# Kernel tuning notes

Hardware: AMD Instinct MI355X
Metric: run time of the kernel (lower is better)

Reference implementation:

```python
import jax, jax.numpy as jnp
import numpy as np

H = 16      # query heads
KV = 4      # kv heads
HD = 128    # head dim
THETA = 10000.0
NEG = -1e9


def _rope_tables(S, dtype):
    inv_freq = 1.0 / (THETA ** (jnp.arange(0, HD, 2, dtype=jnp.float32) / HD))
    ang = jnp.arange(S, dtype=jnp.float32)[:, None] * inv_freq[None, :]  # [S, HD/2]
    emb = jnp.concatenate([ang, ang], axis=-1)  # [S, HD]
    return jnp.cos(emb).astype(dtype), jnp.sin(emb).astype(dtype)


def _rotate_half(x):
    x1, x2 = jnp.split(x, 2, axis=-1)
    return jnp.concatenate([-x2, x1], axis=-1)


def _apply_rope(t, cos, sin):
    # t: [B, h, S, HD]; cos/sin: [S, HD]
    return t * cos[None, None] + _rotate_half(t) * sin[None, None]


def setup_inputs() -> dict:
    key = jax.random.key(0)
    ks = jax.random.split(key, 5)
    B, S, D = 2, 2048, 2048
    sc = 0.02
    return {
        "x": jax.random.normal(ks[0], (B, S, D), jnp.float32),
        "wq": jax.random.normal(ks[1], (D, D), jnp.float32) * sc,
        "wk": jax.random.normal(ks[2], (KV * HD, D), jnp.float32) * sc,
        "wv": jax.random.normal(ks[3], (KV * HD, D), jnp.float32) * sc,
        "wo": jax.random.normal(ks[4], (D, D), jnp.float32) * sc,
    }


def reference(x, wq, wk, wv, wo):
    B, S, D = x.shape
    q = (x @ wq.T).reshape(B, S, H, HD).transpose(0, 2, 1, 3)   # [B,H,S,HD]
    k = (x @ wk.T).reshape(B, S, KV, HD).transpose(0, 2, 1, 3)  # [B,KV,S,HD]
    v = (x @ wv.T).reshape(B, S, KV, HD).transpose(0, 2, 1, 3)

    cos, sin = _rope_tables(S, x.dtype)
    q = _apply_rope(q, cos, sin)
    k = _apply_rope(k, cos, sin)

    # GQA: repeat kv heads to match query heads (q_group_num = H // KV)
    k = jnp.repeat(k, H // KV, axis=1)  # [B,H,S,HD]
    v = jnp.repeat(v, H // KV, axis=1)

    scores = jnp.einsum("bhqd,bhkd->bhqk", q, k) / jnp.sqrt(jnp.float32(HD)).astype(x.dtype)
    causal = jnp.where(jnp.tril(jnp.ones((S, S), bool)), 0.0, NEG).astype(jnp.float32)
    attn = jax.nn.softmax(scores.astype(jnp.float32) + causal, axis=-1).astype(x.dtype)

    out = jnp.einsum("bhqk,bhkd->bhqd", attn, v)  # [B,H,S,HD]
    out = out.transpose(0, 2, 1, 3).reshape(B, S, D)
    return out @ wo.T
```

## Files before the change

kernel.cpp:

```cpp
#include <hip/hip_runtime.h>
#include <math.h>

typedef unsigned short u16;
typedef __attribute__((ext_vector_type(8))) short short8;
typedef __attribute__((ext_vector_type(8))) __bf16 bf16x8;
typedef __attribute__((ext_vector_type(4))) float floatx4;
typedef __attribute__((ext_vector_type(16))) float floatx16;
typedef __attribute__((ext_vector_type(4))) unsigned short u16x4;
typedef __attribute__((ext_vector_type(4))) float float4v;
typedef __attribute__((ext_vector_type(4))) unsigned int uint4v;

static __device__ __forceinline__ float b2f(u16 u) {
  unsigned int x = ((unsigned int)u) << 16;
  return __builtin_bit_cast(float, x);
}
static __device__ __forceinline__ u16 f2b(float f) {
  unsigned int x = __builtin_bit_cast(unsigned int, f);
  x += 0x7fffu + ((x >> 16) & 1u);
  return (u16)(x >> 16);
}
static __device__ __forceinline__ unsigned int pk2(float lo, float hi) {
  unsigned int r;
  asm("v_cvt_pk_bf16_f32 %0, %1, %2" : "=v"(r) : "v"(lo), "v"(hi));
  return r;
}
static __device__ __forceinline__ float max3f(float a, float b, float c) {
  return fmaxf(fmaxf(a, b), c);
}
static __device__ __forceinline__ void gload_lds16(const void* g, void* l) {
  __builtin_amdgcn_global_load_lds(
      (const __attribute__((address_space(1))) unsigned int*)g,
      (__attribute__((address_space(3))) unsigned int*)l, 16, 0, 0);
}

__global__ __launch_bounds__(256) void cvt5_kernel(
    const float* __restrict__ x, const float* __restrict__ wq,
    const float* __restrict__ wk, const float* __restrict__ wv,
    const float* __restrict__ wo, u16* __restrict__ xb, u16* __restrict__ wqb,
    u16* __restrict__ wkb, u16* __restrict__ wvb, u16* __restrict__ wob) {
  int bid = blockIdx.x;
  const float* in;
  u16* out;
  int i0;
  if (bid < 8192) { in = x; out = xb; i0 = bid; }
  else if (bid < 12288) { in = wq; out = wqb; i0 = bid - 8192; }
  else if (bid < 13312) { in = wk; out = wkb; i0 = bid - 12288; }
  else if (bid < 14336) { in = wv; out = wvb; i0 = bid - 13312; }
  else { in = wo; out = wob; i0 = bid - 14336; }
  int i = i0 * 256 + threadIdx.x;
  float4v v = reinterpret_cast<const float4v*>(in)[i];
  u16x4 o;
  o[0] = f2b(v[0]); o[1] = f2b(v[1]); o[2] = f2b(v[2]); o[3] = f2b(v[3]);
  reinterpret_cast<u16x4*>(out)[i] = o;
}

__global__ __launch_bounds__(256) void rope_table_kernel(float* __restrict__ ct,
                                                         float* __restrict__ st) {
  int idx = blockIdx.x * 256 + threadIdx.x;
  int s = idx >> 6, j = idx & 63;
  float inv = powf(10000.0f, -(float)j * (1.0f / 64.0f));
  float ang = (float)s * inv;
  ct[idx] = cosf(ang);
  st[idx] = sinf(ang);
}

__global__ __launch_bounds__(256) void kvprep_kernel(const u16* __restrict__ in,
                                                     u16* __restrict__ kr,
                                                     u16* __restrict__ vtb,
                                                     const float* __restrict__ ct,
                                                     const float* __restrict__ st) {
  __shared__ u16 t[128][66];
  if (blockIdx.x < 512) {
    int idx = blockIdx.x * 256 + threadIdx.x;
    int jc = idx & 7;
    int rest = idx >> 3;
    int h = rest & 3;
    int bs = rest >> 2;
    int s = bs & 2047;
    int b = bs >> 11;
    int j0 = jc * 8;
    size_t inoff = (size_t)bs * 3072 + 2048 + h * 128 + j0;
    short8 lo = *reinterpret_cast<const short8*>(&in[inoff]);
    short8 hi = *reinterpret_cast<const short8*>(&in[inoff + 64]);
    short8 o0, o1;
#pragma unroll
    for (int e = 0; e < 8; ++e) {
      float c = ct[s * 64 + j0 + e], sn = st[s * 64 + j0 + e];
      float t1 = b2f((u16)lo[e]);
      float t2 = b2f((u16)hi[e]);
      o0[e] = (short)f2b(t1 * c - t2 * sn);
      o1[e] = (short)f2b(t2 * c + t1 * sn);
    }
    size_t ooff = ((size_t)(b * 4 + h) * 2048 + s) * 128 + j0;
    *reinterpret_cast<short8*>(&kr[ooff]) = o0;
    *reinterpret_cast<short8*>(&kr[ooff + 64]) = o1;
  } else {
    int vb = blockIdx.x - 512;
    int s0 = (vb & 31) * 64;
    int by = vb >> 5;
    int b = by >> 2, kv = by & 3;
    int tid = threadIdx.x;
#pragma unroll
    for (int it = 0; it < 32; ++it) {
      int idx = it * 256 + tid;
      int sl = idx >> 7, d = idx & 127;
      t[d][sl] = in[(size_t)(b * 2048 + s0 + sl) * 3072 + 2560 + kv * 128 + d];
    }
    __syncthreads();
#pragma unroll
    for (int it = 0; it < 32; ++it) {
      int idx = it * 256 + tid;
      int d = idx >> 6, sl = idx & 63;
      vtb[(size_t)((b * 4 + kv) * 128 + d) * 2048 + s0 + sl] = t[d][sl];
    }
  }
}

static __device__ __forceinline__ void store_out(u16* p, float v) { *p = f2b(v); }
static __device__ __forceinline__ void store_out(float* p, float v) { *p = v; }

template <typename OutT>
__global__ __launch_bounds__(256) void gemm_bt(const u16* __restrict__ A,
                                               const u16* __restrict__ B,
                                               OutT* __restrict__ C, int M, int N, int K) {
  __shared__ __align__(16) u16 Al[3][128 * 32];
  __shared__ __align__(16) u16 Bl[3][128 * 32];
  const int tid = threadIdx.x;
  const int lane = tid & 63;
  const int w = tid >> 6;
  const int wr = w >> 1, wc = w & 1;
  const int lr = lane & 15, lg = lane >> 4;
  const int brow = blockIdx.y, bcol = blockIdx.x;
  const int r0 = lane >> 2, kp = lane & 3;
  const u16* Ag = A + (size_t)(brow * 128) * K;
  const u16* Bg = B + (size_t)(bcol * 128) * K;
  floatx4 acc[4][4] = {};
  const int NT = K >> 5;

  auto stage = [&](int buf, int t) {
#pragma unroll
    for (int j = 0; j < 2; ++j) {
      int c = w * 2 + j;
      int row = c * 16 + r0;
      gload_lds16(Ag + (size_t)row * K + t * 32 + kp * 8, &Al[buf][c * 512]);
      gload_lds16(Bg + (size_t)row * K + t * 32 + kp * 8, &Bl[buf][c * 512]);
    }
  };

  stage(0, 0);
  stage(1, 1);
  asm volatile("s_waitcnt vmcnt(4)\n\ts_barrier" ::: "memory");

  int cur = 0, nxt = 2;
  for (int t = 0; t < NT; ++t) {
    if (t + 2 < NT) stage(nxt, t + 2);
    bf16x8 af[4], bfr[4];
#pragma unroll
    for (int m = 0; m < 4; ++m)
      af[m] = *reinterpret_cast<const bf16x8*>(&Al[cur][(wr * 64 + m * 16 + lr) * 32 + lg * 8]);
#pragma unroll
    for (int n = 0; n < 4; ++n)
      bfr[n] = *reinterpret_cast<const bf16x8*>(&Bl[cur][(wc * 64 + n * 16 + lr) * 32 + lg * 8]);
    __builtin_amdgcn_s_setprio(1);
#pragma unroll
    for (int m = 0; m < 4; ++m)
#pragma unroll
      for (int n = 0; n < 4; ++n)
        acc[m][n] = __builtin_amdgcn_mfma_f32_16x16x32_bf16(af[m], bfr[n], acc[m][n], 0, 0, 0);
    __builtin_amdgcn_s_setprio(0);
    if (t + 2 < NT) {
      asm volatile("s_waitcnt vmcnt(4)\n\ts_barrier" ::: "memory");
    } else if (t + 1 < NT) {
      asm volatile("s_waitcnt vmcnt(0)\n\ts_barrier" ::: "memory");
    }
    cur = (cur == 2) ? 0 : cur + 1;
    nxt = (nxt == 2) ? 0 : nxt + 1;
  }
#pragma unroll
  for (int m = 0; m < 4; ++m) {
    int row = brow * 128 + wr * 64 + m * 16 + lg * 4;
#pragma unroll
    for (int n = 0; n < 4; ++n) {
      int col = bcol * 128 + wc * 64 + n * 16 + lr;
#pragma unroll
      for (int i = 0; i < 4; ++i) store_out(&C[(size_t)(row + i) * N + col], acc[m][n][i]);
    }
  }
}

__global__ __launch_bounds__(256, 2) void attn_kernel(
    const u16* __restrict__ QKV, const u16* __restrict__ K,
    const u16* __restrict__ V, const float* __restrict__ ct,
    const float* __restrict__ st, u16* __restrict__ O, u16* __restrict__ Opart,
    float* __restrict__ Mpart, float* __restrict__ Lpart) {
  __shared__ __align__(16) u16 Kl[2][64 * 128];
  __shared__ __align__(16) u16 Vl[2][128 * 64];
  const int tid = threadIdx.x, lane = tid & 63, w = tid >> 6;
  const int ql = lane & 31, h2 = lane >> 5;
  const int idx = blockIdx.x;
  const int bh = idx & 31, pp = (idx >> 5) & 7, half = idx >> 8;
  const int b = bh >> 4, hh = bh & 15, kv = hh >> 2;
  const int t_l = 15 - pp, t_s = pp;
  const int pidx = bh * 8 + pp;
  const u16* Kp = K + (size_t)(b * 4 + kv) * 2048 * 128;
  const u16* Vp = V + (size_t)(b * 4 + kv) * 128 * 2048;
  const float cl = 0.08838834764831845f * 1.44269504088896f;
  const uint4v ones_u = {0x3F803F80u, 0x3F803F80u, 0x3F803F80u, 0x3F803F80u};
  const bf16x8 ones = __builtin_bit_cast(bf16x8, ones_u);

  auto stage = [&](int buf, int kb) {
#pragma unroll
    for (int j = 0; j < 4; ++j) {
      int slot = j * 256 + tid;
      int row = slot >> 4, d16 = slot & 15;
      gload_lds16(Kp + (size_t)(kb * 64 + row) * 128 + (d16 ^ (row & 15)) * 8,
                  &Kl[buf][(j * 256 + w * 64) * 8]);
      int d = slot >> 3, k8 = slot & 7;
      gload_lds16(Vp + (size_t)d * 2048 + kb * 64 + (k8 ^ (d & 7)) * 8,
                  &Vl[buf][(j * 256 + w * 64) * 8]);
    }
  };

  auto run_segment = [&](int t, int kvs, int kve, int part) {
    const int q0w = t * 128 + w * 32;
    const int qg = q0w + ql;
    bf16x8 qa[8];
    {
      const u16* qp = QKV + ((size_t)(b * 2048 + qg)) * 3072 + hh * 128;
      short8 rr[8];
#pragma unroll
      for (int dk = 0; dk < 8; ++dk)
        rr[dk] = *reinterpret_cast<const short8*>(qp + dk * 16 + h2 * 8);
      const float* cb = ct + (size_t)qg * 64;
      const float* sb = st + (size_t)qg * 64;
#pragma unroll
      for (int dk = 0; dk < 4; ++dk) {
        short8 olo, ohi;
#pragma unroll
        for (int e = 0; e < 8; ++e) {
          int j = dk * 16 + h2 * 8 + e;
          float c = cb[j] * cl, sn = sb[j] * cl;
          float t1 = b2f((u16)rr[dk][e]);
          float t2 = b2f((u16)rr[dk + 4][e]);
          olo[e] = (short)f2b(t1 * c - t2 * sn);
          ohi[e] = (short)f2b(t2 * c + t1 * sn);
        }
        qa[dk] = __builtin_bit_cast(bf16x8, olo);
        qa[dk + 4] = __builtin_bit_cast(bf16x8, ohi);
      }
    }
    float m_r = -1e30f;
    floatx16 oacc[4] = {};
    floatx16 lsum = {};
    stage(0, kvs);
    __syncthreads();
    int cur = 0;
    for (int kb = kvs; kb < kve; ++kb) {
      if (kb + 1 < kve) stage(cur ^ 1, kb + 1);
      if (kb * 64 <= q0w + 31) {
        const u16* Klc = Kl[cur];
        const u16* Vlc = Vl[cur];
        floatx16 sT0 = {}, sT1 = {};
        __builtin_amdgcn_s_setprio(1);
#pragma unroll
        for (int dk = 0; dk < 8; ++dk) {
          int row0 = ql, row1 = 32 + ql;
          bf16x8 ak0 = *reinterpret_cast<const bf16x8*>(
              &Klc[row0 * 128 + (((dk * 2 + h2) ^ (row0 & 15))) * 8]);
          bf16x8 ak1 = *reinterpret_cast<const bf16x8*>(
              &Klc[row1 * 128 + (((dk * 2 + h2) ^ (row1 & 15))) * 8]);
          sT0 = __builtin_amdgcn_mfma_f32_32x32x16_bf16(ak0, qa[dk], sT0, 0, 0, 0);
          sT1 = __builtin_amdgcn_mfma_f32_32x32x16_bf16(ak1, qa[dk], sT1, 0, 0, 0);
        }
        __builtin_amdgcn_s_setprio(0);
        float x[32];
        const bool domask = (kb * 64 + 63 > q0w);
#pragma unroll
        for (int rg = 0; rg < 16; ++rg) {
          int kloc0 = (rg & 3) + 8 * (rg >> 2) + 4 * h2;
          float v0 = sT0[rg];
          float v1 = sT1[rg];
          if (domask) {
            if (kb * 64 + kloc0 > qg) v0 = -1e30f;
            if (kb * 64 + 32 + kloc0 > qg) v1 = -1e30f;
          }
          x[rg] = v0;
          x[16 + rg] = v1;
        }
        float mx[16];
#pragma unroll
        for (int i = 0; i < 16; ++i) mx[i] = fmaxf(x[i], x[i + 16]);
        float y0 = max3f(mx[0], mx[1], mx[2]);
        float y1 = max3f(mx[3], mx[4], mx[5]);
        float y2 = max3f(mx[6], mx[7], mx[8]);
        float y3 = max3f(mx[9], mx[10], mx[11]);
        float y4 = max3f(mx[12], mx[13], mx[14]);
        float tmax = fmaxf(max3f(y0, y1, y2), max3f(y3, y4, mx[15]));
        tmax = fmaxf(tmax, __shfl_xor(tmax, 32));
        if (!__all(tmax - m_r <= 11.0f)) {
          float mn = fmaxf(m_r, tmax);
          float al = exp2f(m_r - mn);
          m_r = mn;
#pragma unroll
          for (int rg = 0; rg < 16; ++rg) {
            int rowq = (rg & 3) + 8 * (rg >> 2) + 4 * h2;
            float arow = __shfl(al, rowq);
            oacc[0][rg] *= arow; oacc[1][rg] *= arow;
            oacc[2][rg] *= arow; oacc[3][rg] *= arow;
            lsum[rg] *= arow;
          }
        }
        float p[32];
#pragma unroll
        for (int i = 0; i < 32; ++i) p[i] = exp2f(x[i] - m_r);
        bf16x8 pa[4];
#pragma unroll
        for (int ka = 0; ka < 2; ++ka) {
          const int o = ka * 16;
          unsigned int x0 = pk2(p[o + 0], p[o + 1]);
          unsigned int x1 = pk2(p[o + 2], p[o + 3]);
          unsigned int y0u = pk2(p[o + 4], p[o + 5]);
          unsigned int y1u = pk2(p[o + 6], p[o + 7]);
          asm volatile("v_permlane32_swap_b32 %0, %1" : "+v"(x0), "+v"(y0u));
          asm volatile("v_permlane32_swap_b32 %0, %1" : "+v"(x1), "+v"(y1u));
          uint4v f0 = {x0, x1, y0u, y1u};
          pa[ka * 2] = __builtin_bit_cast(bf16x8, f0);
          unsigned int z0 = pk2(p[o + 8], p[o + 9]);
          unsigned int z1 = pk2(p[o + 10], p[o + 11]);
          unsigned int u0 = pk2(p[o + 12], p[o + 13]);
          unsigned int u1 = pk2(p[o + 14], p[o + 15]);
          asm volatile("v_permlane32_swap_b32 %0, %1" : "+v"(z0), "+v"(u0));
          asm volatile("v_permlane32_swap_b32 %0, %1" : "+v"(z1), "+v"(u1));
          uint4v f1 = {z0, z1, u0, u1};
          pa[ka * 2 + 1] = __builtin_bit_cast(bf16x8, f1);
        }
        __builtin_amdgcn_s_setprio(1);
#pragma unroll
        for (int tb = 0; tb < 4; ++tb) {
          int d = tb * 32 + ql;
#pragma unroll
          for (int ks = 0; ks < 4; ++ks) {
            bf16x8 bv = *reinterpret_cast<const bf16x8*>(
                &Vlc[d * 64 + (((ks * 2 + h2) ^ (d & 7))) * 8]);
            oacc[tb] = __builtin_amdgcn_mfma_f32_32x32x16_bf16(pa[ks], bv, oacc[tb], 0, 0, 0);
          }
        }
#pragma unroll
        for (int ks = 0; ks < 4; ++ks)
          lsum = __builtin_amdgcn_mfma_f32_32x32x16_bf16(pa[ks], ones, lsum, 0, 0, 0);
        __builtin_amdgcn_s_setprio(0);
      }
      __syncthreads();
      cur ^= 1;
    }
    if (part < 0) {
#pragma unroll
      for (int rg = 0; rg < 16; ++rg) {
        int rowq = (rg & 3) + 8 * (rg >> 2) + 4 * h2;
        float inv = 1.0f / lsum[rg];
        int qrow = t * 128 + w * 32 + rowq;
        size_t base = ((size_t)(b * 2048 + qrow)) * 2048 + hh * 128 + ql;
#pragma unroll
        for (int tb = 0; tb < 4; ++tb)
          O[base + tb * 32] = f2b(oacc[tb][rg] * inv);
      }
    } else {
      size_t pb = ((size_t)(part * 256 + pidx)) * 128;
#pragma unroll
      for (int rg = 0; rg < 16; ++rg) {
        int rowq = (rg & 3) + 8 * (rg >> 2) + 4 * h2;
        size_t base = (pb + w * 32 + rowq) * 128 + ql;
#pragma unroll
        for (int tb = 0; tb < 4; ++tb)
          Opart[base + tb * 32] = f2b(oacc[tb][rg]);
      }
      if (h2 == 0) {
        Mpart[pb + w * 32 + ql] = m_r;
      }
      if (ql == 0) {
#pragma unroll
        for (int rg = 0; rg < 16; ++rg) {
          int rowq = (rg & 3) + 8 * (rg >> 2) + 4 * h2;
          Lpart[pb + w * 32 + rowq] = lsum[rg];
        }
      }
    }
  };

  if (half == 0) {
    run_segment(t_l, 0, 17, 0);
  } else {
    run_segment(t_l, 17, 2 * t_l + 2, 1);
    run_segment(t_s, 0, 2 * t_s + 2, -1);
  }
}

__global__ __launch_bounds__(256) void combine_kernel(
    const u16* __restrict__ Opart, const float* __restrict__ Mpart,
    const float* __restrict__ Lpart, u16* __restrict__ O) {
  int pidx = blockIdx.x;
  int bh = pidx >> 3, pp = pidx & 7;
  int b = bh >> 4, hh = bh & 15;
  int t_l = 15 - pp;
  int tid = threadIdx.x;
  int row = tid >> 1, colbase = (tid & 1) * 64;
  size_t pb0 = (size_t)pidx * 128 + row;
  size_t pb1 = (size_t)(256 + pidx) * 128 + row;
  float m0 = Mpart[pb0], m1 = Mpart[pb1];
  float l0 = Lpart[pb0], l1 = Lpart[pb1];
  float M = fmaxf(m0, m1);
  float w0 = exp2f(m0 - M), w1 = exp2f(m1 - M);
  float inv = 1.0f / (w0 * l0 + w1 * l1);
  size_t ob = ((size_t)(b * 2048 + t_l * 128 + row)) * 2048 + hh * 128 + colbase;
#pragma unroll
  for (int k = 0; k < 8; ++k) {
    short8 o0 = *reinterpret_cast<const short8*>(&Opart[pb0 * 128 + colbase + k * 8]);
    short8 o1 = *reinterpret_cast<const short8*>(&Opart[pb1 * 128 + colbase + k * 8]);
    short8 r;
#pragma unroll
    for (int e = 0; e < 8; ++e)
      r[e] = (short)f2b((w0 * b2f((u16)o0[e]) + w1 * b2f((u16)o1[e])) * inv);
    *reinterpret_cast<short8*>(&O[ob + k * 8]) = r;
  }
}

extern "C" void kernel_launch(void* const* d_in, const int* in_sizes, int n_in,
                              void* d_out, int out_size, void* d_ws, size_t ws_size,
                              hipStream_t stream) {
  const float* x  = (const float*)d_in[0];
  const float* wq = (const float*)d_in[1];
  const float* wk = (const float*)d_in[2];
  const float* wv = (const float*)d_in[3];
  const float* wo = (const float*)d_in[4];
  float* out = (float*)d_out;
  char* ws = (char*)d_ws;
  size_t off = 0;
  auto alloc = [&](size_t bytes) -> void* {
    void* p = ws + off;
    off = (off + bytes + 255) & ~(size_t)255;
    return p;
  };
  u16* xb   = (u16*)alloc(4096ull * 2048 * 2);
  u16* wqb  = (u16*)alloc(2048ull * 2048 * 2);
  u16* wkb  = (u16*)alloc(512ull * 2048 * 2);
  u16* wvb  = (u16*)alloc(512ull * 2048 * 2);
  u16* wob  = (u16*)alloc(2048ull * 2048 * 2);
  u16* qkv  = (u16*)alloc(4096ull * 3072 * 2);
  u16* kr   = (u16*)alloc(4096ull * 512 * 2);
  u16* vtb  = (u16*)alloc(4096ull * 512 * 2);
  float* ctab = (float*)alloc(2048ull * 64 * 4);
  float* stab = (float*)alloc(2048ull * 64 * 4);
  u16* opart  = (u16*)alloc(2ull * 256 * 128 * 128 * 2);
  float* mpart = (float*)alloc(2ull * 256 * 128 * 4);
  float* lpart = (float*)alloc(2ull * 256 * 128 * 4);
  u16* attnb = xb;
  (void)in_sizes; (void)n_in; (void)out_size; (void)ws_size;

  cvt5_kernel<<<18432, 256, 0, stream>>>(x, wq, wk, wv, wo, xb, wqb, wkb, wvb, wob);
  rope_table_kernel<<<512, 256, 0, stream>>>(ctab, stab);

  gemm_bt<u16><<<dim3(24, 32), 256, 0, stream>>>(xb, wqb, qkv, 4096, 3072, 2048);

  kvprep_kernel<<<768, 256, 0, stream>>>(qkv, kr, vtb, ctab, stab);

  attn_kernel<<<dim3(512), 256, 0, stream>>>(qkv, kr, vtb, ctab, stab, attnb,
                                             opart, mpart, lpart);
  combine_kernel<<<dim3(256), 256, 0, stream>>>(opart, mpart, lpart, attnb);

  gemm_bt<float><<<dim3(16, 32), 256, 0, stream>>>(attnb, wob, out, 4096, 2048, 2048);
}
```

Measured before the change: 216.9 us.

## Software-pipeline PV MFMA behind next QK and fold rope table into convert kernel

The attention loop now defers the P·V MFMAs of each KV block to the next iteration, so they are issued after the next block's QK^T MFMAs and can overlap the softmax VALU work. V gets a third LDS buffer so the deferred block's V tile stays valid while the next tile is staged. Separately, the rope table computation is merged into the conversion kernel as extra blocks, removing one launch. The cost is more LDS per block (which may reduce occupancy from the requested 2 blocks/CU) and extra registers held for the pending P fragments.

```diff
diff --git a/kernel.cpp b/kernel.cpp
--- a/kernel.cpp
+++ b/kernel.cpp
@@ -37,8 +37,18 @@
     const float* __restrict__ x, const float* __restrict__ wq,
     const float* __restrict__ wk, const float* __restrict__ wv,
     const float* __restrict__ wo, u16* __restrict__ xb, u16* __restrict__ wqb,
-    u16* __restrict__ wkb, u16* __restrict__ wvb, u16* __restrict__ wob) {
+    u16* __restrict__ wkb, u16* __restrict__ wvb, u16* __restrict__ wob,
+    float* __restrict__ ct, float* __restrict__ st) {
   int bid = blockIdx.x;
+  if (bid >= 18432) {
+    int idx = (bid - 18432) * 256 + threadIdx.x;
+    int s = idx >> 6, j = idx & 63;
+    float inv = powf(10000.0f, -(float)j * (1.0f / 64.0f));
+    float ang = (float)s * inv;
+    ct[idx] = cosf(ang);
+    st[idx] = sinf(ang);
+    return;
+  }
   const float* in;
   u16* out;
   int i0;
@@ -52,16 +62,6 @@
   u16x4 o;
   o[0] = f2b(v[0]); o[1] = f2b(v[1]); o[2] = f2b(v[2]); o[3] = f2b(v[3]);
   reinterpret_cast<u16x4*>(out)[i] = o;
-}
-
-__global__ __launch_bounds__(256) void rope_table_kernel(float* __restrict__ ct,
-                                                         float* __restrict__ st) {
-  int idx = blockIdx.x * 256 + threadIdx.x;
-  int s = idx >> 6, j = idx & 63;
-  float inv = powf(10000.0f, -(float)j * (1.0f / 64.0f));
-  float ang = (float)s * inv;
-  ct[idx] = cosf(ang);
-  st[idx] = sinf(ang);
 }
 
 __global__ __launch_bounds__(256) void kvprep_kernel(const u16* __restrict__ in,
@@ -194,7 +194,7 @@
     const float* __restrict__ st, u16* __restrict__ O, u16* __restrict__ Opart,
     float* __restrict__ Mpart, float* __restrict__ Lpart) {
   __shared__ __align__(16) u16 Kl[2][64 * 128];
-  __shared__ __align__(16) u16 Vl[2][128 * 64];
+  __shared__ __align__(16) u16 Vl[3][128 * 64];
   const int tid = threadIdx.x, lane = tid & 63, w = tid >> 6;
   const int ql = lane & 31, h2 = lane >> 5;
   const int idx = blockIdx.x;
@@ -208,16 +208,18 @@
   const uint4v ones_u = {0x3F803F80u, 0x3F803F80u, 0x3F803F80u, 0x3F803F80u};
   const bf16x8 ones = __builtin_bit_cast(bf16x8, ones_u);
 
-  auto stage = [&](int buf, int kb) {
+  auto stage = [&](int kb) {
+    u16* KlB = Kl[kb & 1];
+    u16* VlB = Vl[kb % 3];
 #pragma unroll
     for (int j = 0; j < 4; ++j) {
       int slot = j * 256 + tid;
       int row = slot >> 4, d16 = slot & 15;
       gload_lds16(Kp + (size_t)(kb * 64 + row) * 128 + (d16 ^ (row & 15)) * 8,
-                  &Kl[buf][(j * 256 + w * 64) * 8]);
+                  &KlB[(j * 256 + w * 64) * 8]);
       int d = slot >> 3, k8 = slot & 7;
       gload_lds16(Vp + (size_t)d * 2048 + kb * 64 + (k8 ^ (d & 7)) * 8,
-                  &Vl[buf][(j * 256 + w * 64) * 8]);
+                  &VlB[(j * 256 + w * 64) * 8]);
     }
   };
 
@@ -252,15 +254,36 @@
     float m_r = -1e30f;
     floatx16 oacc[4] = {};
     floatx16 lsum = {};
-    stage(0, kvs);
+    bf16x8 paP[4];
+    bool have_prev = false;
+    int vprev = 0;
+
+    auto pv_apply = [&](const u16* Vlc) {
+      __builtin_amdgcn_s_setprio(1);
+#pragma unroll
+      for (int tb = 0; tb < 4; ++tb) {
+        int d = tb * 32 + ql;
+#pragma unroll
+        for (int ks = 0; ks < 4; ++ks) {
+          bf16x8 bv = *reinterpret_cast<const bf16x8*>(
+              &Vlc[d * 64 + (((ks * 2 + h2) ^ (d & 7))) * 8]);
+          oacc[tb] = __builtin_amdgcn_mfma_f32_32x32x16_bf16(paP[ks], bv, oacc[tb], 0, 0, 0);
+        }
+      }
+#pragma unroll
+      for (int ks = 0; ks < 4; ++ks)
+        lsum = __builtin_amdgcn_mfma_f32_32x32x16_bf16(paP[ks], ones, lsum, 0, 0, 0);
+      __builtin_amdgcn_s_setprio(0);
+    };
+
+    stage(kvs);
     __syncthreads();
-    int cur = 0;
     for (int kb = kvs; kb < kve; ++kb) {
-      if (kb + 1 < kve) stage(cur ^ 1, kb + 1);
-      if (kb * 64 <= q0w + 31) {
-        const u16* Klc = Kl[cur];
-        const u16* Vlc = Vl[cur];
-        floatx16 sT0 = {}, sT1 = {};
+      if (kb + 1 < kve) stage(kb + 1);
+      const bool doCur = (kb * 64 <= q0w + 31);
+      floatx16 sT0 = {}, sT1 = {};
+      if (doCur) {
+        const u16* Klc = Kl[kb & 1];
         __builtin_amdgcn_s_setprio(1);
 #pragma unroll
         for (int dk = 0; dk < 8; ++dk) {
@@ -273,6 +296,9 @@
           sT1 = __builtin_amdgcn_mfma_f32_32x32x16_bf16(ak1, qa[dk], sT1, 0, 0, 0);
         }
         __builtin_amdgcn_s_setprio(0);
+      }
+      if (have_prev) pv_apply(Vl[vprev]);
+      if (doCur) {
         float x[32];
         const bool domask = (kb * 64 + 63 > q0w);
 #pragma unroll
@@ -313,7 +339,6 @@
         float p[32];
 #pragma unroll
         for (int i = 0; i < 32; ++i) p[i] = exp2f(x[i] - m_r);
-        bf16x8 pa[4];
 #pragma unroll
         for (int ka = 0; ka < 2; ++ka) {
           const int o = ka * 16;
@@ -324,7 +349,7 @@
           asm volatile("v_permlane32_swap_b32 %0, %1" : "+v"(x0), "+v"(y0u));
           asm volatile("v_permlane32_swap_b32 %0, %1" : "+v"(x1), "+v"(y1u));
           uint4v f0 = {x0, x1, y0u, y1u};
-          pa[ka * 2] = __builtin_bit_cast(bf16x8, f0);
+          paP[ka * 2] = __builtin_bit_cast(bf16x8, f0);
           unsigned int z0 = pk2(p[o + 8], p[o + 9]);
           unsigned int z1 = pk2(p[o + 10], p[o + 11]);
           unsigned int u0 = pk2(p[o + 12], p[o + 13]);
@@ -332,27 +357,16 @@
           asm volatile("v_permlane32_swap_b32 %0, %1" : "+v"(z0), "+v"(u0));
           asm volatile("v_permlane32_swap_b32 %0, %1" : "+v"(z1), "+v"(u1));
           uint4v f1 = {z0, z1, u0, u1};
-          pa[ka * 2 + 1] = __builtin_bit_cast(bf16x8, f1);
-        }
-        __builtin_amdgcn_s_setprio(1);
-#pragma unroll
-        for (int tb = 0; tb < 4; ++tb) {
-          int d = tb * 32 + ql;
-#pragma unroll
-          for (int ks = 0; ks < 4; ++ks) {
-            bf16x8 bv = *reinterpret_cast<const bf16x8*>(
-                &Vlc[d * 64 + (((ks * 2 + h2) ^ (d & 7))) * 8]);
-            oacc[tb] = __builtin_amdgcn_mfma_f32_32x32x16_bf16(pa[ks], bv, oacc[tb], 0, 0, 0);
-          }
-        }
-#pragma unroll
-        for (int ks = 0; ks < 4; ++ks)
-          lsum = __builtin_amdgcn_mfma_f32_32x32x16_bf16(pa[ks], ones, lsum, 0, 0, 0);
-        __builtin_amdgcn_s_setprio(0);
-      }
+          paP[ka * 2 + 1] = __builtin_bit_cast(bf16x8, f1);
+        }
+        vprev = kb % 3;
+      }
+      have_prev = doCur;
       __syncthreads();
-      cur ^= 1;
-    }
+    }
+    if (have_prev) pv_apply(Vl[vprev]);
+    __syncthreads();
+
     if (part < 0) {
 #pragma unroll
       for (int rg = 0; rg < 16; ++rg) {
@@ -456,8 +470,8 @@
   u16* attnb = xb;
   (void)in_sizes; (void)n_in; (void)out_size; (void)ws_size;
 
-  cvt5_kernel<<<18432, 256, 0, stream>>>(x, wq, wk, wv, wo, xb, wqb, wkb, wvb, wob);
-  rope_table_kernel<<<512, 256, 0, stream>>>(ctab, stab);
+  cvt5_kernel<<<18944, 256, 0, stream>>>(x, wq, wk, wv, wo, xb, wqb, wkb, wvb, wob,
+                                         ctab, stab);
 
   gemm_bt<u16><<<dim3(24, 32), 256, 0, stream>>>(xb, wqb, qkv, 4096, 3072, 2048);
 
```

New measurement: 217.0 us. About the same (+0.1%).
